# Optimization experiments

Hardware: AMD Instinct MI355X
Metric: run time of the kernel (lower is better)

## Reference

```python
import jax, jax.numpy as jnp
import numpy as np

B, C, H, W = 16, 64, 64, 64
HW = H * W            # = dim = 4096
R = 4                 # reduction_ratio
NH = 8                # head_num
EPS = 1e-5


def setup_inputs() -> dict:
    key = jax.random.key(0)
    ks = jax.random.split(key, 8)
    s = 0.02  # weight init scale
    return {
        "x": jax.random.normal(ks[0], (B, C, H, W), jnp.float32),
        "ln1_w": jnp.ones((C,), jnp.float32),
        "ln1_b": jnp.zeros((C,), jnp.float32),
        "ln2_w": jnp.ones((C,), jnp.float32),
        "ln2_b": jnp.zeros((C,), jnp.float32),
        "W_rk": jax.random.normal(ks[1], (C * R, C), jnp.float32) * s,
        "W_rv": jax.random.normal(ks[2], (C * R, C), jnp.float32) * s,
        "W_q": jax.random.normal(ks[3], (HW, HW), jnp.float32) * s,
        "W_k": jax.random.normal(ks[4], (HW // R, HW // R), jnp.float32) * s,
        "W_v": jax.random.normal(ks[5], (HW // R, HW // R), jnp.float32) * s,
        "W_o": jax.random.normal(ks[6], (HW, HW), jnp.float32) * s,
    }


def _ln(x, w, b):
    # LayerNorm over last axis
    mu = jnp.mean(x, axis=-1, keepdims=True)
    var = jnp.mean((x - mu) ** 2, axis=-1, keepdims=True)
    return (x - mu) / jnp.sqrt(var + EPS) * w + b


def reference(x, ln1_w, ln1_b, ln2_w, ln2_b, W_rk, W_rv, W_q, W_k, W_v, W_o):
    b, c, h, w = x.shape
    hw = h * w
    # ln1: LayerNorm2d == per-pixel LayerNorm over channels
    xn = _ln(x.transpose(0, 2, 3, 1), ln1_w, ln1_b)      # [B,H,W,C]
    xf = xn.reshape(b, hw, c)                            # [B,HW,C] (row-major HW)
    # K/V spatial reduction: 'a (cd r) b -> a cd (b r)'
    kv = xf.reshape(b, hw // R, R, c).transpose(0, 1, 3, 2).reshape(b, hw // R, c * R)
    k = _ln(kv @ W_rk, ln2_w, ln2_b)                     # [B,HW/R,C]
    v = _ln(kv @ W_rv, ln2_w, ln2_b)                     # [B,HW/R,C]
    # projections over the SPATIAL axis (dim = HW)
    q = xf.transpose(0, 2, 1) @ W_q                      # [B,C,HW]
    k = k.transpose(0, 2, 1) @ W_k                       # [B,C,HW/R]
    v = v.transpose(0, 2, 1) @ W_v                       # [B,C,HW/R]
    Lq = hw // NH
    Lk = (hw // R) // NH
    # split heads along spatial axis, attend over channel dim C
    qh = q.reshape(b, c, NH, Lq).transpose(0, 2, 3, 1)   # [B,h,Lq,C]
    kh = k.reshape(b, c, NH, Lk).transpose(0, 2, 3, 1)   # [B,h,Lk,C]
    vh = v.reshape(b, c, NH, Lk).transpose(0, 2, 3, 1)   # [B,h,Lk,C]
    scale = float(hw // NH) ** 0.5
    attn = jax.nn.softmax(jnp.einsum('bhqc,bhkc->bhqk', qh, kh) / scale, axis=-1)
    # dropout is identity at inference
    o = jnp.einsum('bhqk,bhkc->bhqc', attn, vh)          # [B,h,Lq,C]
    # concat_head: heads become outer blocks of the spatial axis
    o = o.transpose(0, 3, 1, 2).reshape(b, c, hw)        # [B,C,HW]
    o = o @ W_o                                          # [B,C,HW]
    return o.reshape(b, c, h, w) + x
```

## Files before the change

kernel.cpp:

```cpp
#include <hip/hip_runtime.h>

typedef unsigned short u16;
typedef unsigned int u32;
typedef __attribute__((ext_vector_type(8))) __bf16 bf16x8;
typedef __attribute__((ext_vector_type(4))) float f32x4;
typedef __attribute__((ext_vector_type(4))) unsigned int u32x4;

#define MFMA16(a, b, c) __builtin_amdgcn_mfma_f32_16x16x32_bf16((a), (b), (c), 0, 0, 0)

__device__ __forceinline__ u16 f2bf(float f) {
  unsigned u = __float_as_uint(f);
  u += 0x7FFFu + ((u >> 16) & 1u);
  return (u16)(u >> 16);
}

typedef __attribute__((address_space(1))) const unsigned char gU8;
typedef __attribute__((address_space(3))) unsigned char sU8;
__device__ __forceinline__ void gload16(const void* g, void* l) {
  __builtin_amdgcn_global_load_lds((gU8*)g, (sU8*)l, 16, 0, 0);
}

__device__ __forceinline__ void wt_body(const float* __restrict__ W, u16* __restrict__ Wt,
                                        int K, int N, int bid, float* tile) {
  int ntn = N >> 6;
  int kt = bid / ntn, nt = bid % ntn;
  int t = threadIdx.x;
  const float* src = W + (size_t)kt * 64 * N + (size_t)nt * 64;
#pragma unroll
  for (int i = 0; i < 4; ++i) {
    int idx = t + i * 256, row = idx >> 4, c4 = idx & 15;
    f32x4 v = *(const f32x4*)&src[(size_t)row * N + c4 * 4];
#pragma unroll
    for (int j = 0; j < 4; ++j) tile[row * 65 + c4 * 4 + j] = v[j];
  }
  __syncthreads();
  u16* dst = Wt + (size_t)nt * 64 * K + (size_t)kt * 64;
#pragma unroll
  for (int i = 0; i < 2; ++i) {
    int idx = t + i * 256, nn = idx >> 3, k8 = idx & 7;
    u16 o[8];
#pragma unroll
    for (int j = 0; j < 8; ++j) o[j] = f2bf(tile[(k8 * 8 + j) * 65 + nn]);
    u32x4 pk;
#pragma unroll
    for (int j = 0; j < 4; ++j) pk[j] = (u32)o[2 * j] | ((u32)o[2 * j + 1] << 16);
    *(u32x4*)&dst[(size_t)nn * K + k8 * 8] = pk;
  }
}

__device__ __forceinline__ void wperm_body(const float* __restrict__ Wrk, const float* __restrict__ Wrv,
                                           u16* __restrict__ Wtk, u16* __restrict__ Wtv, int bid) {
  int idx = bid * 256 + threadIdx.x;
  int cp = idx >> 8, f = idx & 255;
  int k = ((f & 63) << 2) | (f >> 6);
  Wtk[idx] = f2bf(Wrk[k * 64 + cp]);
  Wtv[idx] = f2bf(Wrv[k * 64 + cp]);
}

__device__ __forceinline__ void ln1_body(const float* __restrict__ x, const float* __restrict__ w,
                                         const float* __restrict__ bias, u16* __restrict__ xf_pc,
                                         u16* __restrict__ xfT, int bid, float* tile) {
  int b = bid >> 6, p0 = (bid & 63) << 6;
  int t = threadIdx.x;
  const float* xb = x + (size_t)b * 64 * 4096;
#pragma unroll
  for (int i = 0; i < 4; ++i) {
    int idx = t + i * 256, c = idx >> 4, p4 = idx & 15;
    f32x4 v = *(const f32x4*)&xb[(size_t)c * 4096 + p0 + p4 * 4];
#pragma unroll
    for (int j = 0; j < 4; ++j) tile[c * 65 + p4 * 4 + j] = v[j];
  }
  __syncthreads();
  int lane = t & 63, wv = t >> 6;
  float gw = w[lane], gb = bias[lane];
  for (int pi = 0; pi < 16; ++pi) {
    int p = wv * 16 + pi;
    float v = tile[lane * 65 + p];
    float s = v, s2 = v * v;
#pragma unroll
    for (int m = 1; m < 64; m <<= 1) { s += __shfl_xor(s, m); s2 += __shfl_xor(s2, m); }
    float mean = s * (1.0f / 64.0f);
    float var = s2 * (1.0f / 64.0f) - mean * mean;
    float y = (v - mean) * rsqrtf(var + 1e-5f) * gw + gb;
    tile[lane * 65 + p] = y;
  }
  __syncthreads();
  u16* xfb = xf_pc + (size_t)b * 4096 * 64;
  u16* xtb = xfT + (size_t)b * 64 * 4096;
#pragma unroll
  for (int i = 0; i < 2; ++i) {
    int idx = t + i * 256, p = idx >> 3, c8 = idx & 7;
    u16 o[8];
#pragma unroll
    for (int j = 0; j < 8; ++j) o[j] = f2bf(tile[(c8 * 8 + j) * 65 + p]);
    u32x4 pk;
#pragma unroll
    for (int j = 0; j < 4; ++j) pk[j] = (u32)o[2 * j] | ((u32)o[2 * j + 1] << 16);
    *(u32x4*)&xfb[(size_t)(p0 + p) * 64 + c8 * 8] = pk;
  }
#pragma unroll
  for (int i = 0; i < 2; ++i) {
    int idx = t + i * 256, c = idx >> 3, p8 = idx & 7;
    u16 o[8];
#pragma unroll
    for (int j = 0; j < 8; ++j) o[j] = f2bf(tile[c * 65 + p8 * 8 + j]);
    u32x4 pk;
#pragma unroll
    for (int j = 0; j < 4; ++j) pk[j] = (u32)o[2 * j] | ((u32)o[2 * j + 1] << 16);
    *(u32x4*)&xtb[(size_t)c * 4096 + p0 + p8 * 8] = pk;
  }
}

__global__ __launch_bounds__(256) void prep_kernel(
    const float* __restrict__ W_q, u16* __restrict__ Wt_q,
    const float* __restrict__ W_o, u16* __restrict__ Wt_o,
    const float* __restrict__ W_k, u16* __restrict__ Wt_k,
    const float* __restrict__ W_v, u16* __restrict__ Wt_v,
    const float* __restrict__ W_rk, const float* __restrict__ W_rv,
    u16* __restrict__ Wt_rk, u16* __restrict__ Wt_rv,
    const float* __restrict__ x, const float* __restrict__ ln1w, const float* __restrict__ ln1b,
    u16* __restrict__ xf_pc, u16* __restrict__ xfT) {
  __shared__ float tile[64 * 65];
  int bid = blockIdx.x;
  if (bid < 4096)       wt_body(W_q, Wt_q, 4096, 4096, bid, tile);
  else if (bid < 8192)  wt_body(W_o, Wt_o, 4096, 4096, bid - 4096, tile);
  else if (bid < 8448)  wt_body(W_k, Wt_k, 1024, 1024, bid - 8192, tile);
  else if (bid < 8704)  wt_body(W_v, Wt_v, 1024, 1024, bid - 8448, tile);
  else if (bid < 8768)  wperm_body(W_rk, W_rv, Wt_rk, Wt_rv, bid - 8704);
  else                  ln1_body(x, ln1w, ln1b, xf_pc, xfT, bid - 8768, tile);
}

__global__ __launch_bounds__(256) void kv_kernel(const u16* __restrict__ xf_pc,
                                                 const u16* __restrict__ Wtk, const u16* __restrict__ Wtv,
                                                 const float* __restrict__ ln2w, const float* __restrict__ ln2b,
                                                 u16* __restrict__ kT, u16* __restrict__ vT) {
  __shared__ __align__(16) u16 As[64 * 264];
  __shared__ __align__(16) u16 Bk[64 * 264];
  __shared__ __align__(16) u16 Bv[64 * 264];
  u16* Tk = As;
  u16* Tv = As + 64 * 72;
  int b = blockIdx.x >> 4, s0 = (blockIdx.x & 15) << 6;
  int t = threadIdx.x;
  const u16* Asrc = xf_pc + (size_t)b * 4096 * 64 + (size_t)s0 * 256;
#pragma unroll
  for (int i = 0; i < 8; ++i) {
    int id = t + i * 256, row = id >> 5, c16 = id & 31;
    *(u32x4*)&As[row * 264 + c16 * 8] = *(const u32x4*)&Asrc[(size_t)row * 256 + c16 * 8];
    *(u32x4*)&Bk[row * 264 + c16 * 8] = *(const u32x4*)&Wtk[(size_t)row * 256 + c16 * 8];
    *(u32x4*)&Bv[row * 264 + c16 * 8] = *(const u32x4*)&Wtv[(size_t)row * 256 + c16 * 8];
  }
  __syncthreads();
  int lane = t & 63, wv = t >> 6, lo = lane & 15, hi = lane >> 4;
  f32x4 acck[4] = {}, accv[4] = {};
  int arow = (wv * 16 + lo) * 264 + hi * 8;
#pragma unroll
  for (int kk = 0; kk < 8; ++kk) {
    bf16x8 a = *(const bf16x8*)&As[arow + kk * 32];
#pragma unroll
    for (int nf = 0; nf < 4; ++nf) {
      bf16x8 bk = *(const bf16x8*)&Bk[(nf * 16 + lo) * 264 + kk * 32 + hi * 8];
      bf16x8 bv = *(const bf16x8*)&Bv[(nf * 16 + lo) * 264 + kk * 32 + hi * 8];
      acck[nf] = MFMA16(a, bk, acck[nf]);
      accv[nf] = MFMA16(a, bv, accv[nf]);
    }
  }
  __syncthreads();
  float w2[4], b2[4];
#pragma unroll
  for (int nf = 0; nf < 4; ++nf) { w2[nf] = ln2w[nf * 16 + lo]; b2[nf] = ln2b[nf * 16 + lo]; }
#pragma unroll
  for (int r = 0; r < 4; ++r) {
    float sk = 0.f, sk2 = 0.f, sv = 0.f, sv2 = 0.f;
#pragma unroll
    for (int nf = 0; nf < 4; ++nf) {
      float a = acck[nf][r], c = accv[nf][r];
      sk += a; sk2 += a * a; sv += c; sv2 += c * c;
    }
#pragma unroll
    for (int m = 1; m < 16; m <<= 1) {
      sk += __shfl_xor(sk, m); sk2 += __shfl_xor(sk2, m);
      sv += __shfl_xor(sv, m); sv2 += __shfl_xor(sv2, m);
    }
    float mk = sk * (1.f / 64.f), vk = sk2 * (1.f / 64.f) - mk * mk, rk = rsqrtf(vk + 1e-5f);
    float mv = sv * (1.f / 64.f), vv = sv2 * (1.f / 64.f) - mv * mv, rv = rsqrtf(vv + 1e-5f);
    int srow = wv * 16 + hi * 4 + r;
#pragma unroll
    for (int nf = 0; nf < 4; ++nf) {
      Tk[(nf * 16 + lo) * 72 + srow] = f2bf((acck[nf][r] - mk) * rk * w2[nf] + b2[nf]);
      Tv[(nf * 16 + lo) * 72 + srow] = f2bf((accv[nf][r] - mv) * rv * w2[nf] + b2[nf]);
    }
  }
  __syncthreads();
  u16* kdst = kT + (size_t)b * 64 * 1024 + s0;
  u16* vdst = vT + (size_t)b * 64 * 1024 + s0;
#pragma unroll
  for (int i = 0; i < 16; ++i) {
    int idx = t + i * 256, cp = idx >> 6, s = idx & 63;
    kdst[(size_t)cp * 1024 + s] = Tk[cp * 72 + s];
    vdst[(size_t)cp * 1024 + s] = Tv[cp * 72 + s];
  }
}

__device__ __forceinline__ void stage_tile(const u16* Ab, const u16* Bb, int K, int kt,
                                           u16* As, u16* Bs, int wv, int lane) {
  int gr = lane >> 3;
  int gcol = (lane & 7) * 8;
  const u16* a0 = Ab + (size_t)kt * 64 + gcol;
  const u16* b0 = Bb + (size_t)kt * 64 + gcol;
#pragma unroll
  for (int i = 0; i < 4; ++i) {
    int chunk = wv * 4 + i;
    int row = chunk * 8 + gr;
    gload16(a0 + (size_t)row * K, As + chunk * 512);
    gload16(b0 + (size_t)row * K, Bs + chunk * 512);
  }
}

__device__ __forceinline__ void compute_tile(const u16* As, const u16* Bs, f32x4 acc[4][4],
                                             int wm, int wn, int lo, int hi) {
#pragma unroll
  for (int kk = 0; kk < 2; ++kk) {
    bf16x8 a[4], bb[4];
#pragma unroll
    for (int i = 0; i < 4; ++i) {
      a[i]  = *(const bf16x8*)&As[(wm + i * 16 + lo) * 64 + kk * 32 + hi * 8];
      bb[i] = *(const bf16x8*)&Bs[(wn + i * 16 + lo) * 64 + kk * 32 + hi * 8];
    }
#pragma unroll
    for (int mi = 0; mi < 4; ++mi)
#pragma unroll
      for (int ni = 0; ni < 4; ++ni)
        acc[mi][ni] = MFMA16(a[mi], bb[ni], acc[mi][ni]);
  }
}

template <int EPI>
__device__ void gemm_body(const u16* __restrict__ A, const u16* __restrict__ Bm,
                          void* __restrict__ Cc, const float* __restrict__ resid,
                          int N, int K, int chunkStride, int mt, int nt, u16* lds) {
  int t = threadIdx.x, lane = t & 63, wv = t >> 6;
  int wm = (wv >> 1) * 64, wn = (wv & 1) * 64;
  int lo = lane & 15, hi = lane >> 4;
  f32x4 acc[4][4] = {};
  const u16* Ab = A + (size_t)mt * 128 * K;
  const u16* Bb = Bm + (size_t)nt * 128 * K;
  int nk = K >> 6;
  u16* As0 = lds;          u16* Bs0 = lds + 8192;
  u16* As1 = lds + 16384;  u16* Bs1 = lds + 24576;
  stage_tile(Ab, Bb, K, 0, As0, Bs0, wv, lane);
  __syncthreads();
  for (int kt = 0; kt < nk; kt += 2) {
    stage_tile(Ab, Bb, K, kt + 1, As1, Bs1, wv, lane);
    compute_tile(As0, Bs0, acc, wm, wn, lo, hi);
    __syncthreads();
    if (kt + 2 < nk) stage_tile(Ab, Bb, K, kt + 2, As0, Bs0, wv, lane);
    compute_tile(As1, Bs1, acc, wm, wn, lo, hi);
    __syncthreads();
  }
#pragma unroll
  for (int mi = 0; mi < 4; ++mi)
#pragma unroll
    for (int ni = 0; ni < 4; ++ni)
#pragma unroll
      for (int r = 0; r < 4; ++r) {
        int m = mt * 128 + wm + mi * 16 + hi * 4 + r;
        int n = nt * 128 + wn + ni * 16 + lo;
        float v = acc[mi][ni][r];
        if constexpr (EPI == 0) {
          ((u16*)Cc)[(size_t)m * N + n] = f2bf(v);
        } else if constexpr (EPI == 1) {
          ((u16*)Cc)[(size_t)(n >> 6) * chunkStride + (size_t)m * 64 + (n & 63)] = f2bf(v);
        } else {
          size_t ad = (size_t)m * N + n;
          ((float*)Cc)[ad] = v + resid[ad];
        }
      }
}

template <int EPI>
__global__ __launch_bounds__(256) void gemm_kernel(const u16* __restrict__ A, const u16* __restrict__ Bm,
                                                   void* __restrict__ Cc, const float* __restrict__ resid,
                                                   int N, int K, int chunkStride) {
  __shared__ __align__(16) u16 lds[32768];
  int ntn = N >> 7;
  gemm_body<EPI>(A, Bm, Cc, resid, N, K, chunkStride, blockIdx.x / ntn, blockIdx.x % ntn, lds);
}

__global__ __launch_bounds__(256) void qkv_kernel(
    const u16* __restrict__ Wt_q, const u16* __restrict__ xfT, u16* __restrict__ q_t,
    const u16* __restrict__ Wt_k, const u16* __restrict__ k_lnT, u16* __restrict__ kproj,
    const u16* __restrict__ v_lnT, const u16* __restrict__ Wt_v, u16* __restrict__ vproj) {
  __shared__ __align__(16) u16 lds[32768];
  int bid = blockIdx.x;
  if (bid < 256) {
    gemm_body<1>(Wt_q, xfT, q_t, nullptr, 1024, 4096, 4096 * 64, bid >> 3, bid & 7, lds);
  } else if (bid < 320) {
    int id = bid - 256;
    gemm_body<1>(Wt_k, k_lnT, kproj, nullptr, 1024, 1024, 1024 * 64, id >> 3, id & 7, lds);
  } else {
    int id = bid - 320;
    gemm_body<0>(v_lnT, Wt_v, vproj, nullptr, 1024, 1024, 0, id >> 3, id & 7, lds);
  }
}

__global__ __launch_bounds__(256) void attn_kernel(const u16* __restrict__ q, const u16* __restrict__ kp,
                                                   const u16* __restrict__ vp, u16* __restrict__ o2) {
  __shared__ __align__(16) u16 Qs[128 * 72];
  __shared__ __align__(16) u16 Ks[128 * 72];
  __shared__ __align__(16) u16 Vs[64 * 136];
  __shared__ __align__(16) u16 Ps[128 * 136];
  int qt = blockIdx.x & 3, h = (blockIdx.x >> 2) & 7, b = blockIdx.x >> 5;
  int t = threadIdx.x, lane = t & 63, wv = t >> 6;
  int lo = lane & 15, hi = lane >> 4;
  const u16* qsrc = q + (size_t)b * 4096 * 64 + (size_t)(h * 512 + qt * 128) * 64;
  const u16* ksrc = kp + (size_t)b * 1024 * 64 + (size_t)(h * 128) * 64;
  const u16* vsrc = vp + (size_t)b * 64 * 1024 + h * 128;
#pragma unroll
  for (int i = 0; i < 4; ++i) {
    int id = t + i * 256;
    int row = id >> 3, c16 = id & 7;
    *(u32x4*)&Qs[row * 72 + c16 * 8] = *(const u32x4*)&qsrc[(size_t)row * 64 + c16 * 8];
    *(u32x4*)&Ks[row * 72 + c16 * 8] = *(const u32x4*)&ksrc[(size_t)row * 64 + c16 * 8];
    int vrow = id >> 4, v16 = id & 15;
    *(u32x4*)&Vs[vrow * 136 + v16 * 8] = *(const u32x4*)&vsrc[(size_t)vrow * 1024 + v16 * 8];
  }
  __syncthreads();
  f32x4 s[2][8] = {};
#pragma unroll
  for (int kk = 0; kk < 2; ++kk) {
    bf16x8 a0 = *(const bf16x8*)&Qs[(wv * 32 + lo) * 72 + kk * 32 + hi * 8];
    bf16x8 a1 = *(const bf16x8*)&Qs[(wv * 32 + 16 + lo) * 72 + kk * 32 + hi * 8];
#pragma unroll
    for (int ni = 0; ni < 8; ++ni) {
      bf16x8 bb = *(const bf16x8*)&Ks[(ni * 16 + lo) * 72 + kk * 32 + hi * 8];
      s[0][ni] = MFMA16(a0, bb, s[0][ni]);
      s[1][ni] = MFMA16(a1, bb, s[1][ni]);
    }
  }
  const float inv_scale = 0.044194173824159216f;
#pragma unroll
  for (int mi = 0; mi < 2; ++mi)
#pragma unroll
    for (int ni = 0; ni < 8; ++ni) s[mi][ni] *= inv_scale;
#pragma unroll
  for (int mi = 0; mi < 2; ++mi) {
#pragma unroll
    for (int r = 0; r < 4; ++r) {
      float mx = -1e30f;
#pragma unroll
      for (int ni = 0; ni < 8; ++ni) mx = fmaxf(mx, s[mi][ni][r]);
#pragma unroll
      for (int m = 1; m < 16; m <<= 1) mx = fmaxf(mx, __shfl_xor(mx, m));
      float p[8], sum = 0.f;
#pragma unroll
      for (int ni = 0; ni < 8; ++ni) { p[ni] = __expf(s[mi][ni][r] - mx); sum += p[ni]; }
#pragma unroll
      for (int m = 1; m < 16; m <<= 1) sum += __shfl_xor(sum, m);
      float rs = 1.0f / sum;
      int row = wv * 32 + mi * 16 + hi * 4 + r;
#pragma unroll
      for (int ni = 0; ni < 8; ++ni) Ps[row * 136 + ni * 16 + lo] = f2bf(p[ni] * rs);
    }
  }
  __syncthreads();
  f32x4 o[4][2] = {};
#pragma unroll
  for (int kk = 0; kk < 4; ++kk) {
    bf16x8 b0 = *(const bf16x8*)&Ps[(wv * 32 + lo) * 136 + kk * 32 + hi * 8];
    bf16x8 b1 = *(const bf16x8*)&Ps[(wv * 32 + 16 + lo) * 136 + kk * 32 + hi * 8];
#pragma unroll
    for (int mi = 0; mi < 4; ++mi) {
      bf16x8 a = *(const bf16x8*)&Vs[(mi * 16 + lo) * 136 + kk * 32 + hi * 8];
      o[mi][0] = MFMA16(a, b0, o[mi][0]);
      o[mi][1] = MFMA16(a, b1, o[mi][1]);
    }
  }
  u16* od = o2 + (size_t)b * 64 * 4096 + h * 512 + qt * 128;
#pragma unroll
  for (int mi = 0; mi < 4; ++mi)
#pragma unroll
    for (int ni = 0; ni < 2; ++ni)
#pragma unroll
      for (int r = 0; r < 4; ++r) {
        int c = mi * 16 + hi * 4 + r;
        int lq = wv * 32 + ni * 16 + lo;
        od[(size_t)c * 4096 + lq] = f2bf(o[mi][ni][r]);
      }
}

extern "C" void kernel_launch(void* const* d_in, const int* in_sizes, int n_in,
                              void* d_out, int out_size, void* d_ws, size_t ws_size,
                              hipStream_t stream) {
  (void)in_sizes; (void)n_in; (void)out_size; (void)ws_size;
  const float* x    = (const float*)d_in[0];
  const float* ln1w = (const float*)d_in[1];
  const float* ln1b = (const float*)d_in[2];
  const float* ln2w = (const float*)d_in[3];
  const float* ln2b = (const float*)d_in[4];
  const float* W_rk = (const float*)d_in[5];
  const float* W_rv = (const float*)d_in[6];
  const float* W_q  = (const float*)d_in[7];
  const float* W_k  = (const float*)d_in[8];
  const float* W_v  = (const float*)d_in[9];
  const float* W_o  = (const float*)d_in[10];

  char* ws = (char*)d_ws;
  size_t off = 0;
  auto alloc = [&](size_t bytes) { char* p = ws + off; off += bytes; return p; };
  u16* Wt_q  = (u16*)alloc(4096ull * 4096 * 2);
  u16* Wt_o  = (u16*)alloc(4096ull * 4096 * 2);
  u16* Wt_k  = (u16*)alloc(1024ull * 1024 * 2);
  u16* Wt_v  = (u16*)alloc(1024ull * 1024 * 2);
  u16* Wt_rk = (u16*)alloc(64ull * 256 * 2);
  u16* Wt_rv = (u16*)alloc(64ull * 256 * 2);
  u16* xf_pc = (u16*)alloc(16ull * 4096 * 64 * 2);
  u16* xfT   = (u16*)alloc(16ull * 64 * 4096 * 2);
  u16* k_lnT = (u16*)alloc(16ull * 64 * 1024 * 2);
  u16* v_lnT = (u16*)alloc(16ull * 64 * 1024 * 2);
  u16* q_t   = (u16*)alloc(16ull * 4096 * 64 * 2);
  u16* kproj = (u16*)alloc(16ull * 1024 * 64 * 2);
  u16* vproj = (u16*)alloc(16ull * 64 * 1024 * 2);
  u16* o2    = (u16*)alloc(16ull * 64 * 4096 * 2);

  prep_kernel<<<9792, 256, 0, stream>>>(W_q, Wt_q, W_o, Wt_o, W_k, Wt_k, W_v, Wt_v,
                                        W_rk, W_rv, Wt_rk, Wt_rv, x, ln1w, ln1b, xf_pc, xfT);
  kv_kernel<<<256, 256, 0, stream>>>(xf_pc, Wt_rk, Wt_rv, ln2w, ln2b, k_lnT, v_lnT);
  qkv_kernel<<<384, 256, 0, stream>>>(Wt_q, xfT, q_t, Wt_k, k_lnT, kproj, v_lnT, Wt_v, vproj);
  attn_kernel<<<512, 256, 0, stream>>>(q_t, kproj, vproj, o2);
  gemm_kernel<2><<<256, 256, 0, stream>>>(o2, Wt_o, (float*)d_out, x, 4096, 4096, 0);
}
```

Baseline: 204.2 us.

## Split-K the Q and output GEMMs to raise block count and occupancy

The Q projection is split into 4 K-chunks and the output projection into 2, which raises the grids from 256 to 1024 and 512 GEMM blocks. LDS double buffering is dropped so each block uses half the shared memory, allowing 3 blocks per CU. Partial sums are stored as bf16 and reduced later: Q partials inside the attention kernel's load, output partials in a new reduce kernel that also adds the residual. This trades extra partial-sum memory traffic, an extra launch, bf16 rounding of partials and lost load/compute overlap for better CU utilisation.

```diff
diff --git a/kernel.cpp b/kernel.cpp
--- a/kernel.cpp
+++ b/kernel.cpp
@@ -236,25 +236,20 @@
 
 template <int EPI>
 __device__ void gemm_body(const u16* __restrict__ A, const u16* __restrict__ Bm,
-                          void* __restrict__ Cc, const float* __restrict__ resid,
-                          int N, int K, int chunkStride, int mt, int nt, u16* lds) {
+                          u16* __restrict__ Cc, int N, int K, int chunkStride,
+                          int mt, int nt, int koff, int nk, u16* lds) {
   int t = threadIdx.x, lane = t & 63, wv = t >> 6;
   int wm = (wv >> 1) * 64, wn = (wv & 1) * 64;
   int lo = lane & 15, hi = lane >> 4;
   f32x4 acc[4][4] = {};
-  const u16* Ab = A + (size_t)mt * 128 * K;
-  const u16* Bb = Bm + (size_t)nt * 128 * K;
-  int nk = K >> 6;
-  u16* As0 = lds;          u16* Bs0 = lds + 8192;
-  u16* As1 = lds + 16384;  u16* Bs1 = lds + 24576;
-  stage_tile(Ab, Bb, K, 0, As0, Bs0, wv, lane);
-  __syncthreads();
-  for (int kt = 0; kt < nk; kt += 2) {
-    stage_tile(Ab, Bb, K, kt + 1, As1, Bs1, wv, lane);
-    compute_tile(As0, Bs0, acc, wm, wn, lo, hi);
+  const u16* Ab = A + (size_t)mt * 128 * K + koff;
+  const u16* Bb = Bm + (size_t)nt * 128 * K + koff;
+  u16* As = lds;
+  u16* Bs = lds + 8192;
+  for (int kt = 0; kt < nk; ++kt) {
+    stage_tile(Ab, Bb, K, kt, As, Bs, wv, lane);
     __syncthreads();
-    if (kt + 2 < nk) stage_tile(Ab, Bb, K, kt + 2, As0, Bs0, wv, lane);
-    compute_tile(As1, Bs1, acc, wm, wn, lo, hi);
+    compute_tile(As, Bs, acc, wm, wn, lo, hi);
     __syncthreads();
   }
 #pragma unroll
@@ -267,43 +262,67 @@
         int n = nt * 128 + wn + ni * 16 + lo;
         float v = acc[mi][ni][r];
         if constexpr (EPI == 0) {
-          ((u16*)Cc)[(size_t)m * N + n] = f2bf(v);
-        } else if constexpr (EPI == 1) {
-          ((u16*)Cc)[(size_t)(n >> 6) * chunkStride + (size_t)m * 64 + (n & 63)] = f2bf(v);
+          Cc[(size_t)m * N + n] = f2bf(v);
         } else {
-          size_t ad = (size_t)m * N + n;
-          ((float*)Cc)[ad] = v + resid[ad];
+          Cc[(size_t)(n >> 6) * chunkStride + (size_t)m * 64 + (n & 63)] = f2bf(v);
         }
       }
 }
 
-template <int EPI>
-__global__ __launch_bounds__(256) void gemm_kernel(const u16* __restrict__ A, const u16* __restrict__ Bm,
-                                                   void* __restrict__ Cc, const float* __restrict__ resid,
-                                                   int N, int K, int chunkStride) {
-  __shared__ __align__(16) u16 lds[32768];
-  int ntn = N >> 7;
-  gemm_body<EPI>(A, Bm, Cc, resid, N, K, chunkStride, blockIdx.x / ntn, blockIdx.x % ntn, lds);
-}
-
-__global__ __launch_bounds__(256) void qkv_kernel(
+__global__ __launch_bounds__(256, 3) void qkv_kernel(
     const u16* __restrict__ Wt_q, const u16* __restrict__ xfT, u16* __restrict__ q_t,
     const u16* __restrict__ Wt_k, const u16* __restrict__ k_lnT, u16* __restrict__ kproj,
     const u16* __restrict__ v_lnT, const u16* __restrict__ Wt_v, u16* __restrict__ vproj) {
-  __shared__ __align__(16) u16 lds[32768];
+  __shared__ __align__(16) u16 lds[16384];
   int bid = blockIdx.x;
-  if (bid < 256) {
-    gemm_body<1>(Wt_q, xfT, q_t, nullptr, 1024, 4096, 4096 * 64, bid >> 3, bid & 7, lds);
-  } else if (bid < 320) {
-    int id = bid - 256;
-    gemm_body<1>(Wt_k, k_lnT, kproj, nullptr, 1024, 1024, 1024 * 64, id >> 3, id & 7, lds);
+  if (bid < 1024) {
+    int log = (bid & 7) * 128 + (bid >> 3);
+    int kh = log >> 8, tile = log & 255, mt = tile >> 3, nt = tile & 7;
+    gemm_body<1>(Wt_q, xfT, q_t + (size_t)kh * 4194304, 1024, 4096, 4096 * 64,
+                 mt, nt, kh * 1024, 16, lds);
+  } else if (bid < 1088) {
+    int id = bid - 1024;
+    gemm_body<1>(Wt_k, k_lnT, kproj, 1024, 1024, 1024 * 64, id >> 3, id & 7, 0, 16, lds);
   } else {
-    int id = bid - 320;
-    gemm_body<0>(v_lnT, Wt_v, vproj, nullptr, 1024, 1024, 0, id >> 3, id & 7, lds);
-  }
-}
-
-__global__ __launch_bounds__(256) void attn_kernel(const u16* __restrict__ q, const u16* __restrict__ kp,
+    int id = bid - 1088;
+    gemm_body<0>(v_lnT, Wt_v, vproj, 1024, 1024, 0, id >> 3, id & 7, 0, 16, lds);
+  }
+}
+
+__global__ __launch_bounds__(256, 3) void ogemm_kernel(const u16* __restrict__ o2,
+                                                       const u16* __restrict__ Wt_o,
+                                                       u16* __restrict__ o_part) {
+  __shared__ __align__(16) u16 lds[16384];
+  int bid = blockIdx.x;
+  int log = (bid & 7) * 64 + (bid >> 3);
+  int kh = log >> 8, tile = log & 255, mt = tile >> 5, nt = tile & 31;
+  gemm_body<0>(o2, Wt_o, o_part + (size_t)kh * 4194304, 4096, 4096, 0,
+               mt, nt, kh * 2048, 32, lds);
+}
+
+__global__ __launch_bounds__(256) void oreduce_kernel(const float* __restrict__ x,
+                                                      const u16* __restrict__ p0,
+                                                      const u16* __restrict__ p1,
+                                                      float* __restrict__ out) {
+  size_t base = ((size_t)blockIdx.x * 256 + threadIdx.x) * 8;
+  u32x4 a = *(const u32x4*)&p0[base];
+  u32x4 b = *(const u32x4*)&p1[base];
+  f32x4 x0 = *(const f32x4*)&x[base];
+  f32x4 x1 = *(const f32x4*)&x[base + 4];
+  float r[8];
+#pragma unroll
+  for (int j = 0; j < 4; ++j) {
+    r[2 * j]     = __uint_as_float(a[j] << 16) + __uint_as_float(b[j] << 16);
+    r[2 * j + 1] = __uint_as_float(a[j] & 0xFFFF0000u) + __uint_as_float(b[j] & 0xFFFF0000u);
+  }
+  f32x4 o0, o1;
+#pragma unroll
+  for (int j = 0; j < 4; ++j) { o0[j] = r[j] + x0[j]; o1[j] = r[4 + j] + x1[j]; }
+  *(f32x4*)&out[base] = o0;
+  *(f32x4*)&out[base + 4] = o1;
+}
+
+__global__ __launch_bounds__(256) void attn_kernel(const u16* __restrict__ qp, const u16* __restrict__ kp,
                                                    const u16* __restrict__ vp, u16* __restrict__ o2) {
   __shared__ __align__(16) u16 Qs[128 * 72];
   __shared__ __align__(16) u16 Ks[128 * 72];
@@ -312,14 +331,32 @@
   int qt = blockIdx.x & 3, h = (blockIdx.x >> 2) & 7, b = blockIdx.x >> 5;
   int t = threadIdx.x, lane = t & 63, wv = t >> 6;
   int lo = lane & 15, hi = lane >> 4;
-  const u16* qsrc = q + (size_t)b * 4096 * 64 + (size_t)(h * 512 + qt * 128) * 64;
+  const u16* qsrc = qp + (size_t)b * 262144 + (size_t)(h * 512 + qt * 128) * 64;
   const u16* ksrc = kp + (size_t)b * 1024 * 64 + (size_t)(h * 128) * 64;
   const u16* vsrc = vp + (size_t)b * 64 * 1024 + h * 128;
+#pragma unroll
+  for (int i = 0; i < 4; ++i) {
+    int id = t + i * 256, row = id >> 3, c8 = id & 7;
+    size_t goff = (size_t)row * 64 + c8 * 8;
+    float f[8] = {0.f, 0.f, 0.f, 0.f, 0.f, 0.f, 0.f, 0.f};
+#pragma unroll
+    for (int kh = 0; kh < 4; ++kh) {
+      u32x4 pk = *(const u32x4*)&qsrc[(size_t)kh * 4194304 + goff];
+#pragma unroll
+      for (int j = 0; j < 4; ++j) {
+        f[2 * j]     += __uint_as_float(pk[j] << 16);
+        f[2 * j + 1] += __uint_as_float(pk[j] & 0xFFFF0000u);
+      }
+    }
+    u32x4 pko;
+#pragma unroll
+    for (int j = 0; j < 4; ++j) pko[j] = (u32)f2bf(f[2 * j]) | ((u32)f2bf(f[2 * j + 1]) << 16);
+    *(u32x4*)&Qs[row * 72 + c8 * 8] = pko;
+  }
 #pragma unroll
   for (int i = 0; i < 4; ++i) {
     int id = t + i * 256;
     int row = id >> 3, c16 = id & 7;
-    *(u32x4*)&Qs[row * 72 + c16 * 8] = *(const u32x4*)&qsrc[(size_t)row * 64 + c16 * 8];
     *(u32x4*)&Ks[row * 72 + c16 * 8] = *(const u32x4*)&ksrc[(size_t)row * 64 + c16 * 8];
     int vrow = id >> 4, v16 = id & 15;
     *(u32x4*)&Vs[vrow * 136 + v16 * 8] = *(const u32x4*)&vsrc[(size_t)vrow * 1024 + v16 * 8];
@@ -417,15 +454,17 @@
   u16* xfT   = (u16*)alloc(16ull * 64 * 4096 * 2);
   u16* k_lnT = (u16*)alloc(16ull * 64 * 1024 * 2);
   u16* v_lnT = (u16*)alloc(16ull * 64 * 1024 * 2);
-  u16* q_t   = (u16*)alloc(16ull * 4096 * 64 * 2);
+  u16* q_t   = (u16*)alloc(4ull * 16 * 4096 * 64 * 2);
   u16* kproj = (u16*)alloc(16ull * 1024 * 64 * 2);
   u16* vproj = (u16*)alloc(16ull * 64 * 1024 * 2);
-  u16* o2    = (u16*)alloc(16ull * 64 * 4096 * 2);
+  u16* o2     = xfT;
+  u16* o_part = Wt_q;
 
   prep_kernel<<<9792, 256, 0, stream>>>(W_q, Wt_q, W_o, Wt_o, W_k, Wt_k, W_v, Wt_v,
                                         W_rk, W_rv, Wt_rk, Wt_rv, x, ln1w, ln1b, xf_pc, xfT);
   kv_kernel<<<256, 256, 0, stream>>>(xf_pc, Wt_rk, Wt_rv, ln2w, ln2b, k_lnT, v_lnT);
-  qkv_kernel<<<384, 256, 0, stream>>>(Wt_q, xfT, q_t, Wt_k, k_lnT, kproj, v_lnT, Wt_v, vproj);
+  qkv_kernel<<<1152, 256, 0, stream>>>(Wt_q, xfT, q_t, Wt_k, k_lnT, kproj, v_lnT, Wt_v, vproj);
   attn_kernel<<<512, 256, 0, stream>>>(q_t, kproj, vproj, o2);
-  gemm_kernel<2><<<256, 256, 0, stream>>>(o2, Wt_o, (float*)d_out, x, 4096, 4096, 0);
-}
+  ogemm_kernel<<<512, 256, 0, stream>>>(o2, Wt_o, o_part);
+  oreduce_kernel<<<2048, 256, 0, stream>>>(x, o_part, o_part + 4194304, (float*)d_out);
+}
```

Result: slower. 209.0 us (+2.3%).
